# Kernel optimization log

Measured on AMD Instinct MI355X. Metric: run time of the kernel, lower is better.

Reference implementation:

```python
import jax, jax.numpy as jnp
import numpy as np

N = 12000      # nodes
F = 128        # input feature dim
H = 32         # hidden_dim (hardcoded in module)
TOL = 1e-6     # tolerant_zero_error
AVG_DEG = 32.0


def _glorot(k, shape):
    lim = float(np.sqrt(6.0 / (shape[0] + shape[1])))
    return jax.random.uniform(k, shape, jnp.float32, -lim, lim)


def setup_inputs() -> dict:
    key = jax.random.key(0)
    ks = jax.random.split(key, 8)
    x = jax.random.normal(ks[0], (N, F), jnp.float32)
    # binary sparse-ish adjacency, ~32 neighbors/node, zero diagonal mostly
    a = (jax.random.uniform(ks[1], (N, N)) < (AVG_DEG / N)).astype(jnp.float32)
    W1 = _glorot(ks[2], (2 * F, H)); b1 = jnp.zeros((H,), jnp.float32)
    W2 = _glorot(ks[3], (2 * H, H)); b2 = jnp.zeros((H,), jnp.float32)
    W3 = _glorot(ks[4], (2 * H, H)); b3 = jnp.zeros((H,), jnp.float32)
    Wf1 = _glorot(ks[5], (H, 2 * H)); bf1 = jnp.zeros((2 * H,), jnp.float32)
    Wf2 = _glorot(ks[6], (2 * H, 1)); bf2 = jnp.zeros((1,), jnp.float32)
    return dict(x=x, a=a, W1=W1, b1=b1, W2=W2, b2=b2, W3=W3, b3=b3,
                Wf1=Wf1, bf1=bf1, Wf2=Wf2, bf2=bf2)


def reference(x, a, W1, b1, W2, b2, W3, b3, Wf1, bf1, Wf2, bf2):
    n = a.shape[0]
    idx = jnp.arange(n)
    # add_self_loop: +1 on diagonal entries that are (approximately) zero
    diag = jnp.diagonal(a)
    add = jnp.where(jnp.abs(diag) < TOL, 1.0, 0.0)
    a_hat = a.at[idx, idx].add(add)               # [N, N]
    deg = jnp.sum(a_hat, axis=1, keepdims=True)    # [N, 1], >= 1

    def sage_conv(h, W, b):
        agg = (a_hat @ h) / deg                    # mean neighbor aggregation
        o = jnp.concatenate([h, agg], axis=-1) @ W + b
        # tf.math.l2_normalize(axis=-1) semantics
        o = o / jnp.sqrt(jnp.maximum(jnp.sum(o * o, axis=-1, keepdims=True), 1e-12))
        return jnp.tanh(o)

    h = sage_conv(x, W1, b1)   # [N, 32]
    h = sage_conv(h, W2, b2)   # [N, 32]  (dropout skipped: training=False)
    h = sage_conv(h, W3, b3)   # [N, 32]
    p = jnp.sum(h, axis=0, keepdims=True)          # GlobalSumPool -> [1, 32]
    p = jnp.tanh(p @ Wf1 + bf1)                    # [1, 64]
    return p @ Wf2 + bf2                           # [1, 1]
```

## Files before the change

### kernel.cpp

```cpp
#include <hip/hip_runtime.h>

#define NN 12000
#define FF 128
#define HH 32
#define CAP 96

typedef unsigned int uintv4 __attribute__((ext_vector_type(4)));

__global__ __launch_bounds__(256) void k_scan(const float* __restrict__ a,
                                              unsigned short* __restrict__ adj,
                                              int* __restrict__ deg) {
  const int row = blockIdx.x, tid = threadIdx.x;
  __shared__ int cnt;
  __shared__ unsigned short slist[CAP];
  if (tid == 0) cnt = 0;
  __syncthreads();

  const uintv4* arow = (const uintv4*)(a + (size_t)row * NN);
  uintv4 v[12];
  #pragma unroll
  for (int i = 0; i < 12; ++i) {
    const int c = tid + i * 256;
    uintv4 z = {0u, 0u, 0u, 0u};
    v[i] = (c < NN / 4) ? arow[c] : z;
  }
  #pragma unroll
  for (int i = 0; i < 12; ++i) {
    const int c = tid + i * 256;
    uintv4 w = v[i];
    if ((w.x | w.y | w.z | w.w) == 0u) continue;
    int j0 = 4 * c;
    if (w.x && j0     != row) { int p = atomicAdd(&cnt, 1); if (p < CAP-1) slist[p] = (unsigned short)(j0    ); }
    if (w.y && j0 + 1 != row) { int p = atomicAdd(&cnt, 1); if (p < CAP-1) slist[p] = (unsigned short)(j0 + 1); }
    if (w.z && j0 + 2 != row) { int p = atomicAdd(&cnt, 1); if (p < CAP-1) slist[p] = (unsigned short)(j0 + 2); }
    if (w.w && j0 + 3 != row) { int p = atomicAdd(&cnt, 1); if (p < CAP-1) slist[p] = (unsigned short)(j0 + 3); }
  }
  __syncthreads();
  const int c = min(cnt, CAP - 1);
  if (tid == 0) { slist[c] = (unsigned short)row; deg[row] = c + 1; }
  __syncthreads();
  if (tid < c + 1) adj[(size_t)row * CAP + tid] = slist[tid];
}

__global__ __launch_bounds__(256) void k_sage1(const float* __restrict__ x,
    const float* __restrict__ W, const float* __restrict__ b,
    const unsigned short* __restrict__ adj, const int* __restrict__ deg,
    float* __restrict__ hout) {
  __shared__ float sW[2 * FF * HH];
  __shared__ float sb[HH];
  __shared__ float sbuf[4][2 * FF];
  __shared__ unsigned short sidx[4][CAP];
  const int tid = threadIdx.x;
  for (int i = tid; i < 2 * FF * HH; i += 256) sW[i] = W[i];
  if (tid < HH) sb[tid] = b[tid];

  const int wave = tid >> 6, lane = tid & 63;
  const int node = blockIdx.x * 4 + wave;
  const int d = deg[node];
  for (int n = lane; n < d; n += 64)
    sidx[wave][n] = adj[(size_t)node * CAP + n];
  __syncthreads();

  const float2* x2 = (const float2*)x;
  float a0 = 0.f, a1 = 0.f, b0 = 0.f, b1 = 0.f;
  float c0 = 0.f, c1 = 0.f, e0 = 0.f, e1 = 0.f;
  int n = 0;
  for (; n + 4 <= d; n += 4) {
    int j0 = sidx[wave][n], j1 = sidx[wave][n+1];
    int j2 = sidx[wave][n+2], j3 = sidx[wave][n+3];
    float2 v0 = x2[(size_t)j0 * 64 + lane], v1 = x2[(size_t)j1 * 64 + lane];
    float2 v2 = x2[(size_t)j2 * 64 + lane], v3 = x2[(size_t)j3 * 64 + lane];
    a0 += v0.x; a1 += v0.y;  b0 += v1.x; b1 += v1.y;
    c0 += v2.x; c1 += v2.y;  e0 += v3.x; e1 += v3.y;
  }
  for (; n < d; ++n) {
    float2 vv = x2[(size_t)sidx[wave][n] * 64 + lane];
    a0 += vv.x; a1 += vv.y;
  }
  const float inv = 1.0f / (float)d;
  float s0 = (a0 + b0) + (c0 + e0), s1 = (a1 + b1) + (c1 + e1);
  float2 xi = x2[(size_t)node * 64 + lane];
  sbuf[wave][2 * lane]          = xi.x;
  sbuf[wave][2 * lane + 1]      = xi.y;
  sbuf[wave][FF + 2 * lane]     = s0 * inv;
  sbuf[wave][FF + 2 * lane + 1] = s1 * inv;
  __syncthreads();

  const int k = lane & 31, g = lane >> 5;
  float acc = 0.f;
  const float* bufh = sbuf[wave];
  const int f0 = g * 64;
  #pragma unroll 8
  for (int f = f0; f < f0 + 64; ++f) {
    acc += bufh[f]      * sW[f * HH + k];
    acc += bufh[FF + f] * sW[(FF + f) * HH + k];
  }
  acc += __shfl_xor(acc, 32);
  acc += sb[k];
  float ss = acc * acc;
  for (int off = 16; off; off >>= 1) ss += __shfl_xor(ss, off, 32);
  float r = rsqrtf(fmaxf(ss, 1e-12f));
  if (lane < 32) hout[(size_t)node * HH + k] = tanhf(acc * r);
}

__global__ __launch_bounds__(256) void k_sageh(const float* __restrict__ hin,
    const float* __restrict__ W , const float* __restrict__ b,
    const unsigned short* __restrict__ adj, const int* __restrict__ deg,
    float* __restrict__ hout) {
  __shared__ float sW[2 * HH * HH];
  __shared__ float sb[HH];
  __shared__ float sbuf[4][2 * HH];
  __shared__ unsigned short sidx[4][CAP];
  const int tid = threadIdx.x;
  for (int i = tid; i < 2 * HH * HH; i += 256) sW[i] = W[i];
  if (tid < HH) sb[tid] = b[tid];

  const int wave = tid >> 6, lane = tid & 63;
  const int k = lane & 31, g = lane >> 5;
  const int node = blockIdx.x * 4 + wave;
  const int d = deg[node];
  for (int n = lane; n < d; n += 64)
    sidx[wave][n] = adj[(size_t)node * CAP + n];
  __syncthreads();

  float p0 = 0.f, p1 = 0.f, p2 = 0.f, p3 = 0.f;
  int n = g;
  for (; n + 6 < d; n += 8) {
    p0 += hin[(size_t)sidx[wave][n    ] * HH + k];
    p1 += hin[(size_t)sidx[wave][n + 2] * HH + k];
    p2 += hin[(size_t)sidx[wave][n + 4] * HH + k];
    p3 += hin[(size_t)sidx[wave][n + 6] * HH + k];
  }
  for (; n < d; n += 2)
    p0 += hin[(size_t)sidx[wave][n] * HH + k];
  float agg = (p0 + p1) + (p2 + p3);
  agg += __shfl_xor(agg, 32);
  agg *= 1.0f / (float)d;
  float hi = hin[(size_t)node * HH + k];
  if (g == 0) { sbuf[wave][k] = hi; sbuf[wave][HH + k] = agg; }
  __syncthreads();

  float acc = 0.f;
  const float* bufh = sbuf[wave];
  const int f0 = g * 16;
  #pragma unroll
  for (int f = f0; f < f0 + 16; ++f) {
    acc += bufh[f]      * sW[f * HH + k];
    acc += bufh[HH + f] * sW[(HH + f) * HH + k];
  }
  acc += __shfl_xor(acc, 32);
  acc += sb[k];
  float ss = acc * acc;
  for (int off = 16; off; off >>= 1) ss += __shfl_xor(ss, off, 32);
  float r = rsqrtf(fmaxf(ss, 1e-12f));
  if (lane < 32) hout[(size_t)node * HH + k] = tanhf(acc * r);
}

__global__ __launch_bounds__(256) void k_pool(const float* __restrict__ h3,
                                              float* __restrict__ partial) {
  __shared__ float red[8][HH];
  const int tid = threadIdx.x;
  const int k = tid & 31, c = tid >> 5;
  float s = 0.f;
  for (int node = blockIdx.x * 8 + c; node < NN; node += 64 * 8)
    s += h3[(size_t)node * HH + k];
  red[c][k] = s;
  __syncthreads();
  if (tid < HH) {
    float t = 0.f;
    for (int c2 = 0; c2 < 8; ++c2) t += red[c2][tid];
    partial[blockIdx.x * HH + tid] = t;
  }
}

__global__ __launch_bounds__(64) void k_final(const float* __restrict__ partial,
    const float* __restrict__ Wf1, const float* __restrict__ bf1,
    const float* __restrict__ Wf2, const float* __restrict__ bf2,
    float* __restrict__ out) {
  __shared__ float sp[HH];
  const int lane = threadIdx.x;
  if (lane < HH) {
    float s = 0.f;
    for (int b = 0; b < 64; ++b) s += partial[b * HH + lane];
    sp[lane] = s;
  }
  __syncthreads();
  float q = bf1[lane];
  for (int f = 0; f < HH; ++f) q += sp[f] * Wf1[f * 64 + lane];
  q = tanhf(q);
  float rsum = q * Wf2[lane];
  for (int off = 32; off; off >>= 1) rsum += __shfl_xor(rsum, off);
  if (lane == 0) out[0] = rsum + bf2[0];
}

extern "C" void kernel_launch(void* const* d_in, const int* in_sizes, int n_in,
                              void* d_out, int out_size, void* d_ws, size_t ws_size,
                              hipStream_t stream) {
  const float* x   = (const float*)d_in[0];
  const float* a   = (const float*)d_in[1];
  const float* W1  = (const float*)d_in[2];
  const float* b1  = (const float*)d_in[3];
  const float* W2  = (const float*)d_in[4];
  const float* b2  = (const float*)d_in[5];
  const float* W3  = (const float*)d_in[6];
  const float* b3  = (const float*)d_in[7];
  const float* Wf1 = (const float*)d_in[8];
  const float* bf1 = (const float*)d_in[9];
  const float* Wf2 = (const float*)d_in[10];
  const float* bf2 = (const float*)d_in[11];

  char* ws = (char*)d_ws;
  unsigned short* adj = (unsigned short*)ws;  ws += (size_t)NN * CAP * sizeof(unsigned short);
  int*   deg     = (int*)ws;                  ws += (size_t)((NN * sizeof(int) + 255) & ~(size_t)255);
  float* h1      = (float*)ws;                ws += (size_t)NN * HH * sizeof(float);
  float* h2      = (float*)ws;                ws += (size_t)NN * HH * sizeof(float);
  float* h3      = (float*)ws;                ws += (size_t)NN * HH * sizeof(float);
  float* partial = (float*)ws;

  hipLaunchKernelGGL(k_scan,  dim3(NN),     dim3(256), 0, stream, a, adj, deg);
  hipLaunchKernelGGL(k_sage1, dim3(NN / 4), dim3(256), 0, stream, x,  W1, b1, adj, deg, h1);
  hipLaunchKernelGGL(k_sageh, dim3(NN / 4), dim3(256), 0, stream, h1, W2, b2, adj, deg, h2);
  hipLaunchKernelGGL(k_sageh, dim3(NN / 4), dim3(256), 0, stream, h2, W3, b3, adj, deg, h3);
  hipLaunchKernelGGL(k_pool,  dim3(64),     dim3(256), 0, stream, h3, partial);
  hipLaunchKernelGGL(k_final, dim3(1),      dim3(64),  0, stream, partial, Wf1, bf1, Wf2, bf2, (float*)d_out);
}
```

Baseline: 170.5 us.

## Project layer-1 features before aggregation and fuse pooling into layer 3

Layer 1 now multiplies x by both halves of W1 first (Z = xW_top, Y = xW_bottom), so the neighbour gather reads 32-float rows of Y instead of 128-float rows of x, using linearity of the mean aggregation. The global sum pool is folded into the third SAGE layer through block reductions and atomicAdd into 64 bins, and the bins are zeroed inside the scan kernel. This cuts gather traffic and removes the h3 write and the separate pool kernel, at the cost of an extra kernel and Z/Y buffers, plus nondeterministic float atomics.

```diff
diff --git a/kernel.cpp b/kernel.cpp
--- a/kernel.cpp
+++ b/kernel.cpp
@@ -4,16 +4,21 @@
 #define FF 128
 #define HH 32
 #define CAP 96
+#define NBIN 64
 
 typedef unsigned int uintv4 __attribute__((ext_vector_type(4)));
 
 __global__ __launch_bounds__(256) void k_scan(const float* __restrict__ a,
                                               unsigned short* __restrict__ adj,
-                                              int* __restrict__ deg) {
+                                              int* __restrict__ deg,
+                                              float* __restrict__ partial) {
   const int row = blockIdx.x, tid = threadIdx.x;
   __shared__ int cnt;
   __shared__ unsigned short slist[CAP];
   if (tid == 0) cnt = 0;
+  if (row == 0) {
+    for (int i = tid; i < NBIN * HH; i += 256) partial[i] = 0.f;
+  }
   __syncthreads();
 
   const uintv4* arow = (const uintv4*)(a + (size_t)row * NN);
@@ -42,65 +47,64 @@
   if (tid < c + 1) adj[(size_t)row * CAP + tid] = slist[tid];
 }
 
-__global__ __launch_bounds__(256) void k_sage1(const float* __restrict__ x,
-    const float* __restrict__ W, const float* __restrict__ b,
+__global__ __launch_bounds__(256) void k_xw1(const float* __restrict__ x,
+    const float* __restrict__ W ,
+    float* __restrict__ Z, float* __restrict__ Y) {
+  __shared__ float sW[FF * 64];
+  __shared__ float sx[4][FF];
+  const int tid = threadIdx.x;
+  for (int i = tid; i < FF * 64; i += 256) {
+    int f = i >> 6, k = i & 63;
+    sW[i] = (k < HH) ? W[f * HH + k] : W[(FF + f) * HH + (k - HH)];
+  }
+  const int wave = tid >> 6, lane = tid & 63;
+  const int node = blockIdx.x * 4 + wave;
+  float2 xi = *(const float2*)(x + (size_t)node * FF + lane * 2);
+  __syncthreads();
+  sx[wave][2 * lane] = xi.x;
+  sx[wave][2 * lane + 1] = xi.y;
+  __syncthreads();
+
+  float acc = 0.f;
+  const float* xr = sx[wave];
+  #pragma unroll 8
+  for (int f = 0; f < FF; ++f) acc += xr[f] * sW[f * 64 + lane];
+  if (lane < HH) Z[(size_t)node * HH + lane] = acc;
+  else           Y[(size_t)node * HH + (lane - HH)] = acc;
+}
+
+__global__ __launch_bounds__(256) void k_gl1(const float* __restrict__ Z,
+    const float* __restrict__ Y, const float* __restrict__ b,
     const unsigned short* __restrict__ adj, const int* __restrict__ deg,
     float* __restrict__ hout) {
-  __shared__ float sW[2 * FF * HH];
-  __shared__ float sb[HH];
-  __shared__ float sbuf[4][2 * FF];
   __shared__ unsigned short sidx[4][CAP];
   const int tid = threadIdx.x;
-  for (int i = tid; i < 2 * FF * HH; i += 256) sW[i] = W[i];
-  if (tid < HH) sb[tid] = b[tid];
-
-  const int wave = tid >> 6, lane = tid & 63;
+  const int wave = tid >> 6, lane = tid & 63;
+  const int k = lane & 31, g = lane >> 5;
   const int node = blockIdx.x * 4 + wave;
   const int d = deg[node];
   for (int n = lane; n < d; n += 64)
     sidx[wave][n] = adj[(size_t)node * CAP + n];
   __syncthreads();
 
-  const float2* x2 = (const float2*)x;
-  float a0 = 0.f, a1 = 0.f, b0 = 0.f, b1 = 0.f;
-  float c0 = 0.f, c1 = 0.f, e0 = 0.f, e1 = 0.f;
-  int n = 0;
-  for (; n + 4 <= d; n += 4) {
-    int j0 = sidx[wave][n], j1 = sidx[wave][n+1];
-    int j2 = sidx[wave][n+2], j3 = sidx[wave][n+3];
-    float2 v0 = x2[(size_t)j0 * 64 + lane], v1 = x2[(size_t)j1 * 64 + lane];
-    float2 v2 = x2[(size_t)j2 * 64 + lane], v3 = x2[(size_t)j3 * 64 + lane];
-    a0 += v0.x; a1 += v0.y;  b0 += v1.x; b1 += v1.y;
-    c0 += v2.x; c1 += v2.y;  e0 += v3.x; e1 += v3.y;
-  }
-  for (; n < d; ++n) {
-    float2 vv = x2[(size_t)sidx[wave][n] * 64 + lane];
-    a0 += vv.x; a1 += vv.y;
-  }
-  const float inv = 1.0f / (float)d;
-  float s0 = (a0 + b0) + (c0 + e0), s1 = (a1 + b1) + (c1 + e1);
-  float2 xi = x2[(size_t)node * 64 + lane];
-  sbuf[wave][2 * lane]          = xi.x;
-  sbuf[wave][2 * lane + 1]      = xi.y;
-  sbuf[wave][FF + 2 * lane]     = s0 * inv;
-  sbuf[wave][FF + 2 * lane + 1] = s1 * inv;
-  __syncthreads();
-
-  const int k = lane & 31, g = lane >> 5;
-  float acc = 0.f;
-  const float* bufh = sbuf[wave];
-  const int f0 = g * 64;
-  #pragma unroll 8
-  for (int f = f0; f < f0 + 64; ++f) {
-    acc += bufh[f]      * sW[f * HH + k];
-    acc += bufh[FF + f] * sW[(FF + f) * HH + k];
-  }
-  acc += __shfl_xor(acc, 32);
-  acc += sb[k];
-  float ss = acc * acc;
+  float p0 = 0.f, p1 = 0.f, p2 = 0.f, p3 = 0.f;
+  int n = g;
+  for (; n + 6 < d; n += 8) {
+    p0 += Y[(size_t)sidx[wave][n    ] * HH + k];
+    p1 += Y[(size_t)sidx[wave][n + 2] * HH + k];
+    p2 += Y[(size_t)sidx[wave][n + 4] * HH + k];
+    p3 += Y[(size_t)sidx[wave][n + 6] * HH + k];
+  }
+  for (; n < d; n += 2)
+    p0 += Y[(size_t)sidx[wave][n] * HH + k];
+  float agg = (p0 + p1) + (p2 + p3);
+  agg += __shfl_xor(agg, 32);
+  agg *= 1.0f / (float)d;
+  float o = Z[(size_t)node * HH + k] + agg + b[k];
+  float ss = o * o;
   for (int off = 16; off; off >>= 1) ss += __shfl_xor(ss, off, 32);
   float r = rsqrtf(fmaxf(ss, 1e-12f));
-  if (lane < 32) hout[(size_t)node * HH + k] = tanhf(acc * r);
+  if (lane < 32) hout[(size_t)node * HH + k] = tanhf(o * r);
 }
 
 __global__ __launch_bounds__(256) void k_sageh(const float* __restrict__ hin,
@@ -156,20 +160,62 @@
   if (lane < 32) hout[(size_t)node * HH + k] = tanhf(acc * r);
 }
 
-__global__ __launch_bounds__(256) void k_pool(const float* __restrict__ h3,
-                                              float* __restrict__ partial) {
-  __shared__ float red[8][HH];
-  const int tid = threadIdx.x;
-  const int k = tid & 31, c = tid >> 5;
-  float s = 0.f;
-  for (int node = blockIdx.x * 8 + c; node < NN; node += 64 * 8)
-    s += h3[(size_t)node * HH + k];
-  red[c][k] = s;
+__global__ __launch_bounds__(256) void k_sageh3(const float* __restrict__ hin,
+    const float* __restrict__ W, const float* __restrict__ b,
+    const unsigned short* __restrict__ adj, const int* __restrict__ deg,
+    float* __restrict__ partial) {
+  __shared__ float sW[2 * HH * HH];
+  __shared__ float sb[HH];
+  __shared__ float sbuf[4][2 * HH];
+  __shared__ float red[4][HH];
+  __shared__ unsigned short sidx[4][CAP];
+  const int tid = threadIdx.x;
+  for (int i = tid; i < 2 * HH * HH; i += 256) sW[i] = W[i];
+  if (tid < HH) sb[tid] = b[tid];
+
+  const int wave = tid >> 6, lane = tid & 63;
+  const int k = lane & 31, g = lane >> 5;
+  const int node = blockIdx.x * 4 + wave;
+  const int d = deg[node];
+  for (int n = lane; n < d; n += 64)
+    sidx[wave][n] = adj[(size_t)node * CAP + n];
+  __syncthreads();
+
+  float p0 = 0.f, p1 = 0.f, p2 = 0.f, p3 = 0.f;
+  int n = g;
+  for (; n + 6 < d; n += 8) {
+    p0 += hin[(size_t)sidx[wave][n    ] * HH + k];
+    p1 += hin[(size_t)sidx[wave][n + 2] * HH + k];
+    p2 += hin[(size_t)sidx[wave][n + 4] * HH + k];
+    p3 += hin[(size_t)sidx[wave][n + 6] * HH + k];
+  }
+  for (; n < d; n += 2)
+    p0 += hin[(size_t)sidx[wave][n] * HH + k];
+  float agg = (p0 + p1) + (p2 + p3);
+  agg += __shfl_xor(agg, 32);
+  agg *= 1.0f / (float)d;
+  float hi = hin[(size_t)node * HH + k];
+  if (g == 0) { sbuf[wave][k] = hi; sbuf[wave][HH + k] = agg; }
+  __syncthreads();
+
+  float acc = 0.f;
+  const float* bufh = sbuf[wave];
+  const int f0 = g * 16;
+  #pragma unroll
+  for (int f = f0; f < f0 + 16; ++f) {
+    acc += bufh[f]      * sW[f * HH + k];
+    acc += bufh[HH + f] * sW[(HH + f) * HH + k];
+  }
+  acc += __shfl_xor(acc, 32);
+  acc += sb[k];
+  float ss = acc * acc;
+  for (int off = 16; off; off >>= 1) ss += __shfl_xor(ss, off, 32);
+  float r = rsqrtf(fmaxf(ss, 1e-12f));
+  if (lane < 32) red[wave][k] = tanhf(acc * r);
   __syncthreads();
   if (tid < HH) {
-    float t = 0.f;
-    for (int c2 = 0; c2 < 8; ++c2) t += red[c2][tid];
-    partial[blockIdx.x * HH + tid] = t;
+    float t = (red[0][tid] + red[1][tid]) + (red[2][tid] + red[3][tid]);
+    atomicAdd(&partial[(blockIdx.x & (NBIN - 1)) * HH + tid], t);
   }
 }
 
@@ -181,7 +227,7 @@
   const int lane = threadIdx.x;
   if (lane < HH) {
     float s = 0.f;
-    for (int b = 0; b < 64; ++b) s += partial[b * HH + lane];
+    for (int bb = 0; bb < NBIN; ++bb) s += partial[bb * HH + lane];
     sp[lane] = s;
   }
   __syncthreads();
@@ -212,15 +258,16 @@
   char* ws = (char*)d_ws;
   unsigned short* adj = (unsigned short*)ws;  ws += (size_t)NN * CAP * sizeof(unsigned short);
   int*   deg     = (int*)ws;                  ws += (size_t)((NN * sizeof(int) + 255) & ~(size_t)255);
+  float* Zb      = (float*)ws;                ws += (size_t)NN * HH * sizeof(float);
+  float* Yb      = (float*)ws;                ws += (size_t)NN * HH * sizeof(float);
   float* h1      = (float*)ws;                ws += (size_t)NN * HH * sizeof(float);
   float* h2      = (float*)ws;                ws += (size_t)NN * HH * sizeof(float);
-  float* h3      = (float*)ws;                ws += (size_t)NN * HH * sizeof(float);
   float* partial = (float*)ws;
 
-  hipLaunchKernelGGL(k_scan,  dim3(NN),     dim3(256), 0, stream, a, adj, deg);
-  hipLaunchKernelGGL(k_sage1, dim3(NN / 4), dim3(256), 0, stream, x,  W1, b1, adj, deg, h1);
-  hipLaunchKernelGGL(k_sageh, dim3(NN / 4), dim3(256), 0, stream, h1, W2, b2, adj, deg, h2);
-  hipLaunchKernelGGL(k_sageh, dim3(NN / 4), dim3(256), 0, stream, h2, W3, b3, adj, deg, h3);
-  hipLaunchKernelGGL(k_pool,  dim3(64),     dim3(256), 0, stream, h3, partial);
-  hipLaunchKernelGGL(k_final, dim3(1),      dim3(64),  0, stream, partial, Wf1, bf1, Wf2, bf2, (float*)d_out);
-}
+  hipLaunchKernelGGL(k_scan,   dim3(NN),     dim3(256), 0, stream, a, adj, deg, partial);
+  hipLaunchKernelGGL(k_xw1,    dim3(NN / 4), dim3(256), 0, stream, x, W1, Zb, Yb);
+  hipLaunchKernelGGL(k_gl1,    dim3(NN / 4), dim3(256), 0, stream, Zb, Yb, b1, adj, deg, h1);
+  hipLaunchKernelGGL(k_sageh,  dim3(NN / 4), dim3(256), 0, stream, h1, W2, b2, adj, deg, h2);
+  hipLaunchKernelGGL(k_sageh3, dim3(NN / 4), dim3(256), 0, stream, h2, W3, b3, adj, deg, partial);
+  hipLaunchKernelGGL(k_final,  dim3(1),      dim3(64),  0, stream, partial, Wf1, bf1, Wf2, bf2, (float*)d_out);
+}
```

New measurement: 161.1 us. -5.5%, faster.
